# Optimization experiments

Measured on AMD Instinct MI355X. Metric: run time of the kernel, lower is better.

The kernel has to match this reference:

```python
import jax, jax.numpy as jnp
import numpy as np

B, CI, CO, H, W, E, R, K = 32, 128, 256, 64, 64, 8, 16, 3


def setup_inputs() -> dict:
    key = jax.random.key(0)
    ks = jax.random.split(key, 12)
    def n(k, shape, scale):
        return jax.random.normal(k, shape, dtype=jnp.float32) * scale
    return {
        "x": n(ks[0], (B, CI, H, W), 1.0),
        "experts": n(ks[1], (E, CO, CI, K, K), 0.1),
        # routing SE: C -> C/R -> C -> E (1x1 convs == dense on pooled vec)
        "rw1": n(ks[2], (CI // R, CI), 0.05), "rb1": jnp.zeros((CI // R,), jnp.float32),
        "rw2": n(ks[3], (CI, CI // R), 0.05), "rb2": jnp.zeros((CI,), jnp.float32),
        "rw3": n(ks[4], (E, CI), 0.05),      "rb3": jnp.zeros((E,), jnp.float32),
        # channel attention SE on output: CO -> CO/R -> CO
        "aw1": n(ks[5], (CO // R, CO), 0.05), "ab1": jnp.zeros((CO // R,), jnp.float32),
        "aw2": n(ks[6], (CO, CO // R), 0.05), "ab2": jnp.zeros((CO,), jnp.float32),
    }


def reference(x, experts, rw1, rb1, rw2, rb2, rw3, rb3, aw1, ab1, aw2, ab2):
    # --- routing: SE-style gate -> softmax over experts ---
    pooled = x.mean(axis=(2, 3))                       # [B, CI]
    h = jax.nn.relu(pooled @ rw1.T + rb1)              # [B, CI/R]
    s = jax.nn.sigmoid(h @ rw2.T + rb2)                # [B, CI]
    rweights = jax.nn.softmax(s @ rw3.T + rb3, axis=1) # [B, E]
    # --- per-sample expert kernel combination ---
    w = jnp.einsum('be,eoihw->boihw', rweights, experts)  # [B, CO, CI, K, K]
    # --- per-sample conv (== grouped conv with groups=B) via vmap ---
    def conv1(xi, wi):
        # xi: [CI,H,W], wi: [CO,CI,K,K]
        return jax.lax.conv_general_dilated(
            xi[None], wi, window_strides=(1, 1), padding=[(1, 1), (1, 1)],
            dimension_numbers=('NCHW', 'OIHW', 'NCHW'))[0]
    out = jax.vmap(conv1)(x, w)                        # [B, CO, H, W]
    # --- channel attention on output ---
    p = out.mean(axis=(2, 3))                          # [B, CO]
    ca = jax.nn.sigmoid(jax.nn.relu(p @ aw1.T + ab1) @ aw2.T + ab2)
    return out * ca[:, :, None, None]
```

## Files before the change

kernel.cpp:

```cpp
#include <hip/hip_runtime.h>
#include <hip/hip_bf16.h>


#define BB 32
#define CI_ 128
#define CO_ 256
#define HW_ 4096
#define KK 1152

typedef unsigned short u16;
typedef __attribute__((ext_vector_type(8))) __bf16 bf16x8;
typedef __attribute__((ext_vector_type(4))) float floatx4;

typedef const __attribute__((address_space(1))) void* gptr_t;
typedef __attribute__((address_space(3))) void* sptr_t;

__device__ __forceinline__ void gload_lds16(const void* g, void* s) {
  __builtin_amdgcn_global_load_lds((gptr_t)g, (sptr_t)s, 16, 0, 0);
}

__global__ __launch_bounds__(256) void k_stats2(const float* __restrict__ x,
                                                float* __restrict__ Sr,
                                                float* __restrict__ pooled,
                                                unsigned* __restrict__ zp) {
  int blk = blockIdx.x;
  int tid = threadIdx.x;
  if (blk == 0 && tid < 64) zp[tid] = 0u;
  int b = blk >> 7, ci = blk & 127;
  const float4* xp = (const float4*)(x + ((size_t)(b * CI_ + ci) << 12));
  float T = 0.f, r0 = 0.f, r63 = 0.f, c0 = 0.f, c63 = 0.f;
  __shared__ float corn[4];
  __shared__ float wsum[4][5];
#pragma unroll
  for (int j = 0; j < 4; j++) {
    int idx = j * 256 + tid;
    float4 v = xp[idx];
    float rs = v.x + v.y + v.z + v.w;
    T += rs;
    int x16 = idx & 15;
    if (idx < 16)    r0  += rs;
    if (idx >= 1008) r63 += rs;
    if (x16 == 0)  c0  += v.x;
    if (x16 == 15) c63 += v.w;
    if (idx == 0)    corn[0] = v.x;
    if (idx == 15)   corn[1] = v.w;
    if (idx == 1008) corn[2] = v.x;
    if (idx == 1023) corn[3] = v.w;
  }
  for (int off = 32; off; off >>= 1) {
    T   += __shfl_down(T, off);
    r0  += __shfl_down(r0, off);
    r63 += __shfl_down(r63, off);
    c0  += __shfl_down(c0, off);
    c63 += __shfl_down(c63, off);
  }
  int w = tid >> 6, lane = tid & 63;
  if (lane == 0) { wsum[w][0]=T; wsum[w][1]=r0; wsum[w][2]=r63; wsum[w][3]=c0; wsum[w][4]=c63; }
  __syncthreads();
  if (tid == 0) {
    T   = wsum[0][0]+wsum[1][0]+wsum[2][0]+wsum[3][0];
    r0  = wsum[0][1]+wsum[1][1]+wsum[2][1]+wsum[3][1];
    r63 = wsum[0][2]+wsum[1][2]+wsum[2][2]+wsum[3][2];
    c0  = wsum[0][3]+wsum[1][3]+wsum[2][3]+wsum[3][3];
    c63 = wsum[0][4]+wsum[1][4]+wsum[2][4]+wsum[3][4];
    pooled[b * CI_ + ci] = T * (1.0f / 4096.0f);
#pragma unroll
    for (int ky = 0; ky < 3; ky++) {
#pragma unroll
      for (int kx = 0; kx < 3; kx++) {
        int dy = ky - 1, dx = kx - 1;
        float s = T;
        if (dy == -1) s -= r63;
        if (dy ==  1) s -= r0;
        if (dx == -1) s -= c63;
        if (dx ==  1) s -= c0;
        if (dy != 0 && dx != 0) s += corn[(dy == -1 ? 2 : 0) + (dx == -1 ? 1 : 0)];
        Sr[(b * 9 + ky * 3 + kx) * CI_ + ci] = s * (1.0f / 4096.0f);
      }
    }
  }
}

__global__ __launch_bounds__(256) void k_xform(const float* __restrict__ x,
                                               u16* __restrict__ xt) {
  int blk = blockIdx.x;
  int b = blk >> 6, y = blk & 63;
  __shared__ u16 ts[64][132];
  int tid = threadIdx.x;
  const float* xb = x + ((size_t)b << 19) + (y << 6);
#pragma unroll
  for (int it = 0; it < 8; it++) {
    int idx = it * 256 + tid;
    int ci = idx >> 4, x4 = idx & 15;
    float4 v = *(const float4*)(xb + (size_t)ci * 4096 + x4 * 4);
    __hip_bfloat16 h0 = __float2bfloat16(v.x), h1 = __float2bfloat16(v.y);
    __hip_bfloat16 h2 = __float2bfloat16(v.z), h3 = __float2bfloat16(v.w);
    int xx = x4 << 2;
    ts[xx + 0][ci] = *(const u16*)&h0;
    ts[xx + 1][ci] = *(const u16*)&h1;
    ts[xx + 2][ci] = *(const u16*)&h2;
    ts[xx + 3][ci] = *(const u16*)&h3;
  }
  __syncthreads();
  uint2* ot = (uint2*)(xt + ((size_t)b * HW_ + y * 64) * CI_);
#pragma unroll
  for (int it = 0; it < 8; it++) {
    int o = it * 256 + tid;
    int pix = o >> 5, c4 = o & 31;
    ot[o] = *(const uint2*)&ts[pix][c4 * 4];
  }
}

__global__ __launch_bounds__(128) void k_route2(const float* __restrict__ pooled,
    const float* __restrict__ rw1, const float* __restrict__ rb1,
    const float* __restrict__ rw2, const float* __restrict__ rb2,
    const float* __restrict__ rw3, const float* __restrict__ rb3,
    float* __restrict__ r) {
  int b = blockIdx.x, tid = threadIdx.x;
  int o = tid >> 4, l = tid & 15;
  __shared__ float ps[128], hs[8], ss[128], lg[8];
  ps[tid] = pooled[b * 128 + tid];
  __syncthreads();
  {
    float a = 0.f;
#pragma unroll
    for (int j = 0; j < 8; j++) a += ps[l * 8 + j] * rw1[o * 128 + l * 8 + j];
    a += __shfl_xor(a, 1); a += __shfl_xor(a, 2);
    a += __shfl_xor(a, 4); a += __shfl_xor(a, 8);
    if (l == 0) hs[o] = fmaxf(a + rb1[o], 0.f);
  }
  __syncthreads();
  {
    float a = rb2[tid];
#pragma unroll
    for (int j = 0; j < 8; j++) a += hs[j] * rw2[tid * 8 + j];
    ss[tid] = 1.f / (1.f + expf(-a));
  }
  __syncthreads();
  {
    float a = 0.f;
#pragma unroll
    for (int j = 0; j < 8; j++) a += ss[l * 8 + j] * rw3[o * 128 + l * 8 + j];
    a += __shfl_xor(a, 1); a += __shfl_xor(a, 2);
    a += __shfl_xor(a, 4); a += __shfl_xor(a, 8);
    if (l == 0) lg[o] = a + rb3[o];
  }
  __syncthreads();
  if (tid == 0) {
    float m = lg[0];
    for (int e = 1; e < 8; e++) m = fmaxf(m, lg[e]);
    float s = 0.f, ex[8];
    for (int e = 0; e < 8; e++) { ex[e] = expf(lg[e] - m); s += ex[e]; }
    for (int e = 0; e < 8; e++) r[b * 8 + e] = ex[e] / s;
  }
}

__global__ __launch_bounds__(256) void k_combine2(const float* __restrict__ experts,
                                                  const float* __restrict__ r,
                                                  const float* __restrict__ Sr,
                                                  __hip_bfloat16* __restrict__ wr,
                                                  float* __restrict__ p) {
  int co = blockIdx.x, tid = threadIdx.x;
  __shared__ float els[8][1152];
  __shared__ float rsh[32][8];
  __shared__ float pw[4];
#pragma unroll
  for (int it = 0; it < 9; it++) {
    int f = it * 256 + tid;
    int e = f / 288, q = f - e * 288;
    float4 ev = *(const float4*)(experts + (size_t)e * 294912 + (size_t)co * 1152 + q * 4);
    *(float4*)&els[e][q * 4] = ev;
  }
  rsh[tid >> 3][tid & 7] = r[tid];
  __syncthreads();
  int s = tid >> 7, ci = tid & 127;
  for (int bb = 0; bb < 16; bb++) {
    int b = bb * 2 + s;
    float rv[8];
#pragma unroll
    for (int e = 0; e < 8; e++) rv[e] = rsh[b][e];
    float pacc = 0.f;
    __hip_bfloat16* wrow = wr + (size_t)(b * 256 + co) * KK;
    const float* sb = Sr + b * KK;
#pragma unroll
    for (int k = 0; k < 9; k++) {
      float v = 0.f;
#pragma unroll
      for (int e = 0; e < 8; e++) v += rv[e] * els[e][ci * 9 + k];
      wrow[k * 128 + ci] = __float2bfloat16(v);
      pacc += v * sb[k * 128 + ci];
    }
    for (int off = 32; off; off >>= 1) pacc += __shfl_down(pacc, off);
    if ((tid & 63) == 0) pw[tid >> 6] = pacc;
    __syncthreads();
    if (ci == 0) p[b * 256 + co] = pw[s * 2] + pw[s * 2 + 1];
    __syncthreads();
  }
}

__global__ __launch_bounds__(256) void k_catt2(const float* __restrict__ p,
    const float* __restrict__ aw1, const float* __restrict__ ab1,
    const float* __restrict__ aw2, const float* __restrict__ ab2,
    float* __restrict__ ca) {
  int b = blockIdx.x, tid = threadIdx.x;
  int o = tid >> 4, l = tid & 15;
  __shared__ float ps[256], ts[16];
  ps[tid] = p[b * 256 + tid];
  __syncthreads();
  {
    float a = 0.f;
#pragma unroll
    for (int j = 0; j < 16; j++) a += ps[l * 16 + j] * aw1[o * 256 + l * 16 + j];
    a += __shfl_xor(a, 1); a += __shfl_xor(a, 2);
    a += __shfl_xor(a, 4); a += __shfl_xor(a, 8);
    if (l == 0) ts[o] = fmaxf(a + ab1[o], 0.f);
  }
  __syncthreads();
  float a = ab2[tid];
#pragma unroll
  for (int j = 0; j < 16; j++) a += ts[j] * aw2[tid * 16 + j];
  ca[b * 256 + tid] = 1.f / (1.f + expf(-a));
}

__global__ __launch_bounds__(256) void k_conv(const u16* __restrict__ xt,
                                              const u16* __restrict__ wr,
                                              const float* __restrict__ ca,
                                              const u16* __restrict__ zp,
                                              float* __restrict__ out) {
  int blk = blockIdx.x;
  int rp = blk & 31, coT = (blk >> 5) & 1, b = blk >> 6;
  int y0 = rp * 2;
  int coBase = coT * 128;
  int tid = threadIdx.x;
  int w = tid >> 6, lane = tid & 63;
  int wm = w & 1, wn = w >> 1;
  int quad = lane >> 4, l15 = lane & 15;
  int cl = lane & 3;

  __shared__ __align__(16) u16 As[128 * 32];
  __shared__ __align__(16) u16 Bs[128 * 32];

  const u16* aSrc[2];
  int dstOff[2], chB[2], ylocB[2], xlocB[2];
#pragma unroll
  for (int inst = 0; inst < 2; inst++) {
    int rr = w * 32 + inst * 16 + (lane >> 2);
    int s = (rr ^ (rr >> 2)) & 3;
    int ch = cl ^ s;
    aSrc[inst] = wr + (size_t)(b * 256 + coBase + rr) * KK + ch * 8;
    dstOff[inst] = (w * 32 + inst * 16) * 32 + lane * 8;
    chB[inst] = ch;
    ylocB[inst] = rr >> 6;
    xlocB[inst] = rr & 63;
  }

  int aOff[4], bOff[4];
#pragma unroll
  for (int i = 0; i < 4; i++) {
    int m = wm * 64 + i * 16 + l15;
    aOff[i] = m * 32 + ((quad ^ ((m ^ (m >> 2)) & 3)) << 3);
    int n = wn * 64 + i * 16 + l15;
    bOff[i] = n * 32 + ((quad ^ ((n ^ (n >> 2)) & 3)) << 3);
  }

  floatx4 acc[4][4];
#pragma unroll
  for (int i = 0; i < 4; i++)
#pragma unroll
    for (int j = 0; j < 4; j++) acc[i][j] = floatx4{0.f, 0.f, 0.f, 0.f};

  for (int kidx = 0; kidx < 9; kidx++) {
    int ky = kidx / 3, kx = kidx - ky * 3;
    const u16* bSrc[2];
#pragma unroll
    for (int inst = 0; inst < 2; inst++) {
      int ys = y0 + ylocB[inst] + ky - 1;
      int xs = xlocB[inst] + kx - 1;
      bool valid = ((unsigned)ys < 64u) && ((unsigned)xs < 64u);
      bSrc[inst] = valid ? (xt + ((size_t)(b * HW_ + ys * 64 + xs) << 7) + chB[inst] * 8)
                         : (zp + chB[inst] * 8);
    }
    const u16* aS0 = aSrc[0] + kidx * 128;
    const u16* aS1 = aSrc[1] + kidx * 128;
#pragma unroll
    for (int cib = 0; cib < 4; cib++) {
      __syncthreads();
      gload_lds16(aS0 + cib * 32, &As[dstOff[0]]);
      gload_lds16(aS1 + cib * 32, &As[dstOff[1]]);
      gload_lds16(bSrc[0] + cib * 32, &Bs[dstOff[0]]);
      gload_lds16(bSrc[1] + cib * 32, &Bs[dstOff[1]]);
      __syncthreads();
      bf16x8 af[4], bfv[4];
#pragma unroll
      for (int i = 0; i < 4; i++) af[i] = *(const bf16x8*)&As[aOff[i]];
#pragma unroll
      for (int j = 0; j < 4; j++) bfv[j] = *(const bf16x8*)&Bs[bOff[j]];
#pragma unroll
      for (int i = 0; i < 4; i++)
#pragma unroll
        for (int j = 0; j < 4; j++)
          acc[i][j] = __builtin_amdgcn_mfma_f32_16x16x32_bf16(af[i], bfv[j], acc[i][j], 0, 0, 0);
    }
  }

  float cav[4][4];
#pragma unroll
  for (int i = 0; i < 4; i++)
#pragma unroll
    for (int ri = 0; ri < 4; ri++)
      cav[i][ri] = ca[b * 256 + coBase + wm * 64 + i * 16 + quad * 4 + ri];
#pragma unroll
  for (int i = 0; i < 4; i++) {
#pragma unroll
    for (int j = 0; j < 4; j++) {
      int n = wn * 64 + j * 16 + l15;
      int yy = y0 + (n >> 6), xx = n & 63;
#pragma unroll
      for (int ri = 0; ri < 4; ri++) {
        int co = coBase + wm * 64 + i * 16 + quad * 4 + ri;
        out[((size_t)(b * 256 + co) << 12) + (yy << 6) + xx] = acc[i][j][ri] * cav[i][ri];
      }
    }
  }
}

extern "C" void kernel_launch(void* const* d_in, const int* in_sizes, int n_in,
                              void* d_out, int out_size, void* d_ws, size_t ws_size,
                              hipStream_t stream) {
  const float* x       = (const float*)d_in[0];
  const float* experts = (const float*)d_in[1];
  const float* rw1 = (const float*)d_in[2];
  const float* rb1 = (const float*)d_in[3];
  const float* rw2 = (const float*)d_in[4];
  const float* rb2 = (const float*)d_in[5];
  const float* rw3 = (const float*)d_in[6];
  const float* rb3 = (const float*)d_in[7];
  const float* aw1 = (const float*)d_in[8];
  const float* ab1 = (const float*)d_in[9];
  const float* aw2 = (const float*)d_in[10];
  const float* ab2 = (const float*)d_in[11];

  char* ws = (char*)d_ws;
  u16*   xt     = (u16*)(ws + 0);
  __hip_bfloat16* wr = (__hip_bfloat16*)(ws + 33554432);
  float* Sr     = (float*)(ws + 52428800);
  float* pooled = (float*)(ws + 52576256);
  float* r      = (float*)(ws + 52592640);
  float* p      = (float*)(ws + 52593664);
  float* ca     = (float*)(ws + 52626432);
  u16*   zp     = (u16*)(ws + 52659200);

  k_stats2<<<4096, 256, 0, stream>>>(x, Sr, pooled, (unsigned*)zp);
  k_xform<<<2048, 256, 0, stream>>>(x, xt);
  k_route2<<<32, 128, 0, stream>>>(pooled, rw1, rb1, rw2, rb2, rw3, rb3, r);
  k_combine2<<<256, 256, 0, stream>>>(experts, r, Sr, wr, p);
  k_catt2<<<32, 256, 0, stream>>>(p, aw1, ab1, aw2, ab2, ca);
  k_conv<<<2048, 256, 0, stream>>>(xt, (const u16*)wr, ca, zp, (float*)d_out);
}
```

Before: 332.5 us.

## Widen conv K-tile to 64, remap block order, split combine over batch groups

```diff
diff --git a/kernel.cpp b/kernel.cpp
--- a/kernel.cpp
+++ b/kernel.cpp
@@ -160,7 +160,8 @@
                                                   const float* __restrict__ Sr,
                                                   __hip_bfloat16* __restrict__ wr,
                                                   float* __restrict__ p) {
-  int co = blockIdx.x, tid = threadIdx.x;
+  int co = blockIdx.x & 255, g = blockIdx.x >> 8;
+  int tid = threadIdx.x;
   __shared__ float els[8][1152];
   __shared__ float rsh[32][8];
   __shared__ float pw[4];
@@ -174,8 +175,8 @@
   rsh[tid >> 3][tid & 7] = r[tid];
   __syncthreads();
   int s = tid >> 7, ci = tid & 127;
-  for (int bb = 0; bb < 16; bb++) {
-    int b = bb * 2 + s;
+  for (int bb = 0; bb < 4; bb++) {
+    int b = g * 8 + bb * 2 + s;
     float rv[8];
 #pragma unroll
     for (int e = 0; e < 8; e++) rv[e] = rsh[b][e];
@@ -227,40 +228,44 @@
                                               const float* __restrict__ ca,
                                               const u16* __restrict__ zp,
                                               float* __restrict__ out) {
-  int blk = blockIdx.x;
-  int rp = blk & 31, coT = (blk >> 5) & 1, b = blk >> 6;
+  int id = blockIdx.x;
+  int b = (id & 7) | (((id >> 9) & 3) << 3);
+  int rem = (id >> 3) & 63;
+  int coT = rem >> 5, rp = rem & 31;
   int y0 = rp * 2;
   int coBase = coT * 128;
   int tid = threadIdx.x;
   int w = tid >> 6, lane = tid & 63;
   int wm = w & 1, wn = w >> 1;
   int quad = lane >> 4, l15 = lane & 15;
-  int cl = lane & 3;
-
-  __shared__ __align__(16) u16 As[128 * 32];
-  __shared__ __align__(16) u16 Bs[128 * 32];
-
-  const u16* aSrc[2];
-  int dstOff[2], chB[2], ylocB[2], xlocB[2];
-#pragma unroll
-  for (int inst = 0; inst < 2; inst++) {
-    int rr = w * 32 + inst * 16 + (lane >> 2);
-    int s = (rr ^ (rr >> 2)) & 3;
-    int ch = cl ^ s;
-    aSrc[inst] = wr + (size_t)(b * 256 + coBase + rr) * KK + ch * 8;
-    dstOff[inst] = (w * 32 + inst * 16) * 32 + lane * 8;
-    chB[inst] = ch;
-    ylocB[inst] = rr >> 6;
-    xlocB[inst] = rr & 63;
-  }
-
-  int aOff[4], bOff[4];
+  int cl8 = lane & 7, lr = lane >> 3;
+
+  __shared__ __align__(16) u16 As[128 * 64];
+  __shared__ __align__(16) u16 Bs[128 * 64];
+
+  const u16* aP[4];
+  int dstO[4], chB[4], ylocB[4], xlocB[4];
+#pragma unroll
+  for (int ri = 0; ri < 4; ri++) {
+    int rr = ri * 32 + w * 8 + lr;
+    int c = cl8 ^ (rr & 7);
+    aP[ri] = wr + (size_t)(b * 256 + coBase + rr) * KK + c * 8;
+    dstO[ri] = rr * 64 + cl8 * 8;
+    chB[ri] = c;
+    ylocB[ri] = rr >> 6;
+    xlocB[ri] = rr & 63;
+  }
+
+  int aOff[4][2], bOff[4][2];
 #pragma unroll
   for (int i = 0; i < 4; i++) {
     int m = wm * 64 + i * 16 + l15;
-    aOff[i] = m * 32 + ((quad ^ ((m ^ (m >> 2)) & 3)) << 3);
     int n = wn * 64 + i * 16 + l15;
-    bOff[i] = n * 32 + ((quad ^ ((n ^ (n >> 2)) & 3)) << 3);
+#pragma unroll
+    for (int h = 0; h < 2; h++) {
+      aOff[i][h] = m * 64 + ((((h << 2) | quad) ^ (m & 7)) << 3);
+      bOff[i][h] = n * 64 + ((((h << 2) | quad) ^ (n & 7)) << 3);
+    }
   }
 
   floatx4 acc[4][4];
@@ -271,35 +276,40 @@
 
   for (int kidx = 0; kidx < 9; kidx++) {
     int ky = kidx / 3, kx = kidx - ky * 3;
-    const u16* bSrc[2];
-#pragma unroll
-    for (int inst = 0; inst < 2; inst++) {
-      int ys = y0 + ylocB[inst] + ky - 1;
-      int xs = xlocB[inst] + kx - 1;
+    const u16* bP[4];
+    int bStep[4];
+#pragma unroll
+    for (int ri = 0; ri < 4; ri++) {
+      int ys = y0 + ylocB[ri] + ky - 1;
+      int xs = xlocB[ri] + kx - 1;
       bool valid = ((unsigned)ys < 64u) && ((unsigned)xs < 64u);
-      bSrc[inst] = valid ? (xt + ((size_t)(b * HW_ + ys * 64 + xs) << 7) + chB[inst] * 8)
-                         : (zp + chB[inst] * 8);
-    }
-    const u16* aS0 = aSrc[0] + kidx * 128;
-    const u16* aS1 = aSrc[1] + kidx * 128;
-#pragma unroll
-    for (int cib = 0; cib < 4; cib++) {
+      bP[ri] = valid ? (xt + ((size_t)(b * HW_ + ys * 64 + xs) << 7) + chB[ri] * 8)
+                     : (zp + chB[ri] * 8);
+      bStep[ri] = valid ? 64 : 0;
+    }
+#pragma unroll
+    for (int cib = 0; cib < 2; cib++) {
       __syncthreads();
-      gload_lds16(aS0 + cib * 32, &As[dstOff[0]]);
-      gload_lds16(aS1 + cib * 32, &As[dstOff[1]]);
-      gload_lds16(bSrc[0] + cib * 32, &Bs[dstOff[0]]);
-      gload_lds16(bSrc[1] + cib * 32, &Bs[dstOff[1]]);
+#pragma unroll
+      for (int ri = 0; ri < 4; ri++)
+        gload_lds16(aP[ri] + kidx * 128 + cib * 64, &As[dstO[ri]]);
+#pragma unroll
+      for (int ri = 0; ri < 4; ri++)
+        gload_lds16(bP[ri] + cib * bStep[ri], &Bs[dstO[ri]]);
       __syncthreads();
-      bf16x8 af[4], bfv[4];
-#pragma unroll
-      for (int i = 0; i < 4; i++) af[i] = *(const bf16x8*)&As[aOff[i]];
-#pragma unroll
-      for (int j = 0; j < 4; j++) bfv[j] = *(const bf16x8*)&Bs[bOff[j]];
-#pragma unroll
-      for (int i = 0; i < 4; i++)
-#pragma unroll
-        for (int j = 0; j < 4; j++)
-          acc[i][j] = __builtin_amdgcn_mfma_f32_16x16x32_bf16(af[i], bfv[j], acc[i][j], 0, 0, 0);
+#pragma unroll
+      for (int h = 0; h < 2; h++) {
+        bf16x8 af[4], bfv[4];
+#pragma unroll
+        for (int i = 0; i < 4; i++) af[i] = *(const bf16x8*)&As[aOff[i][h]];
+#pragma unroll
+        for (int j = 0; j < 4; j++) bfv[j] = *(const bf16x8*)&Bs[bOff[j][h]];
+#pragma unroll
+        for (int i = 0; i < 4; i++)
+#pragma unroll
+          for (int j = 0; j < 4; j++)
+            acc[i][j] = __builtin_amdgcn_mfma_f32_16x16x32_bf16(af[i], bfv[j], acc[i][j], 0, 0, 0);
+      }
     }
   }
 
@@ -353,7 +363,7 @@
   k_stats2<<<4096, 256, 0, stream>>>(x, Sr, pooled, (unsigned*)zp);
   k_xform<<<2048, 256, 0, stream>>>(x, xt);
   k_route2<<<32, 128, 0, stream>>>(pooled, rw1, rb1, rw2, rb2, rw3, rb3, r);
-  k_combine2<<<256, 256, 0, stream>>>(experts, r, Sr, wr, p);
+  k_combine2<<<1024, 256, 0, stream>>>(experts, r, Sr, wr, p);
   k_catt2<<<32, 256, 0, stream>>>(p, aw1, ab1, aw2, ab2, ca);
   k_conv<<<2048, 256, 0, stream>>>(xt, (const u16*)wr, ca, zp, (float*)d_out);
 }
```

Result: faster. 309.4 us (-6.9%).
